# Kernel tuning notes

Hardware: AMD Instinct MI355X
Metric: run time of the kernel (lower is better)

Reference implementation:

```python
import jax, jax.numpy as jnp
import numpy as np

B, S, D, H = 2, 1536, 1024, 16
DK = D // H
NEG = -1e9
WEIGHT = 1.0  # undefined global `Weight` in source; treated as scalar 1.0


def setup_inputs() -> dict:
    key = jax.random.key(0)
    ks = jax.random.split(key, 16)
    inp = {
        "query": jax.random.normal(ks[0], (B, S, D), jnp.float32),
        "key": jax.random.normal(ks[1], (B, S, D), jnp.float32),
        "value": jax.random.normal(ks[2], (B, S, D), jnp.float32),
        "mask": jax.random.randint(ks[3], (B, 1, 1, S), 0, 2, jnp.int32),
        "mask1": jax.random.randint(ks[4], (B, 1, S, S), 0, 2, jnp.int32).astype(jnp.float32),
        "Wq": jax.random.normal(ks[5], (D, D), jnp.float32) / np.sqrt(D),
        "bq": jnp.zeros((D,), jnp.float32),
        "Wk": jax.random.normal(ks[6], (D, D), jnp.float32) / np.sqrt(D),
        "bk": jnp.zeros((D,), jnp.float32),
        "Wv": jax.random.normal(ks[7], (D, D), jnp.float32) / np.sqrt(D),
        "bv": jnp.zeros((D,), jnp.float32),
        "Wo": jax.random.normal(ks[8], (D, D), jnp.float32) / np.sqrt(D),
        "bo": jnp.zeros((D,), jnp.float32),
    }
    return inp


def _split_heads(x):
    # [B,S,D] -> [B,H,S,DK]
    return x.reshape(B, S, H, DK).transpose(0, 2, 1, 3)


def reference(query, key, value, mask, mask1, Wq, bq, Wk, bk, Wv, bv, Wo, bo):
    q = _split_heads(query @ Wq.T + bq)
    k = _split_heads(key @ Wk.T + bk)
    v = _split_heads(value @ Wv.T + bv)

    scores = jnp.einsum("bhqd,bhkd->bhqk", q, k) / jnp.sqrt(jnp.float32(DK))
    # softmax of mask1 over the query axis (dim=-2), zeros masked out
    m1 = jnp.where(mask1 == 0, NEG, mask1)
    m1s = jax.nn.softmax(m1, axis=-2)
    scores = (1.0 + m1s * mask1) * scores * WEIGHT
    scores = jnp.where(mask == 0, NEG, scores)
    p = jax.nn.softmax(scores, axis=-1)  # dropout: eval mode (identity)
    x = jnp.einsum("bhqk,bhkd->bhqd", p, v)
    x = x.transpose(0, 2, 1, 3).reshape(B, S, D)
    ret = x @ Wo.T + bo
    return ret, scores
```

## Files before the change

kernel.cpp:

```cpp
#include <hip/hip_runtime.h>
#include <hip/hip_bf16.h>

#define B_ 2
#define S_ 1536
#define D_ 1024
#define H_ 16
#define DK_ 64
#define KW_ 48
#define NT_ 24

#define RET_ELEMS 3145728
#define BITPACK_BLOCKS 18432

typedef __attribute__((ext_vector_type(8))) short short8;
typedef __attribute__((ext_vector_type(8))) unsigned short ushort8v;
typedef __attribute__((ext_vector_type(4))) unsigned short ushort4v;
typedef __attribute__((ext_vector_type(4))) float f32x4;

__device__ __forceinline__ unsigned short bf16_rne(float f) {
    return __builtin_bit_cast(unsigned short, __float2bfloat16(f));
}

struct CvtJobs {
    const float* src[7];
    unsigned short* dst[7];
};

__global__ __launch_bounds__(256) void preproc_kernel(
    const float* __restrict__ mask1, unsigned int* __restrict__ bits,
    float* __restrict__ colsum, CvtJobs j)
{
    const int blk = blockIdx.x;
    if (blk < BITPACK_BLOCKS) {
        if (blk < 12) colsum[blk * 256 + threadIdx.x] = 0.f;
        const size_t gid = (size_t)blk * 256 + threadIdx.x;
        const float v = mask1[gid];
        const unsigned long long bal = __ballot(v != 0.f);
        const int l = threadIdx.x & 63;
        if (l == 0)       bits[gid >> 5] = (unsigned int)bal;
        else if (l == 32) bits[gid >> 5] = (unsigned int)(bal >> 32);
        return;
    }
    int rb = blk - BITPACK_BLOCKS;
    int job, base;
    if (rb < 4608) { job = rb / 1536; base = rb % 1536; }
    else { rb -= 4608; job = 3 + rb / 512; base = rb % 512; }
    const size_t i = ((size_t)base * 256 + threadIdx.x) * 8;
    const float* s = j.src[job] + i;
    float4 f0 = *(const float4*)s;
    float4 f1 = *(const float4*)(s + 4);
    ushort8v u;
    u[0]=bf16_rne(f0.x); u[1]=bf16_rne(f0.y); u[2]=bf16_rne(f0.z); u[3]=bf16_rne(f0.w);
    u[4]=bf16_rne(f1.x); u[5]=bf16_rne(f1.y); u[6]=bf16_rne(f1.z); u[7]=bf16_rne(f1.w);
    *(ushort8v*)(j.dst[job] + i) = u;
}

__global__ void colcount_bits_kernel(const unsigned int* __restrict__ bits, float* __restrict__ colsum) {
    const int b     = blockIdx.x / 6;
    const int chunk = blockIdx.x % 6;
    const int col   = chunk * 256 + threadIdx.x;
    const int q0    = blockIdx.y * 96;
    const int wword = col >> 5, bit = col & 31;
    const unsigned int* p = bits + ((size_t)b * S_ + q0) * KW_ + wword;
    int s = 0;
    #pragma unroll 8
    for (int q = 0; q < 96; ++q) s += (p[(size_t)q * KW_] >> bit) & 1u;
    atomicAdd(&colsum[b * S_ + col], (float)s);
}

struct Proj { const unsigned short* A; const unsigned short* W; const float* bias; unsigned short* C; };

__global__ __launch_bounds__(512) void qkv_gemm_kernel(Proj p0, Proj p1, Proj p2) {
    const int bid = blockIdx.x;
    const int xcd = bid & 7, idx = bid >> 3;
    const int zy = xcd * 9 + (idx >> 3);
    const int bx = idx & 7;
    const int z = zy / 24, by = zy % 24;

    const unsigned short* A = z == 0 ? p0.A    : (z == 1 ? p1.A    : p2.A);
    const unsigned short* W = z == 0 ? p0.W    : (z == 1 ? p1.W    : p2.W);
    const float* bias       = z == 0 ? p0.bias : (z == 1 ? p1.bias : p2.bias);
    unsigned short* C       = z == 0 ? p0.C    : (z == 1 ? p1.C    : p2.C);

    __shared__ unsigned short As[128][72];
    __shared__ unsigned short Bs[128][72];
    const int tid = threadIdx.x;
    const int w = tid >> 6, lane = tid & 63;
    const int g = lane >> 4, c = lane & 15;
    const int wm = w >> 2, wn = w & 3;
    const int m0 = by * 128, n0 = bx * 128;
    const int trow = tid >> 2;
    const int tcol = (tid & 3) * 16;

    f32x4 acc[4][2];
    #pragma unroll
    for (int m = 0; m < 4; ++m)
        #pragma unroll
        for (int n = 0; n < 2; ++n)
            acc[m][n] = f32x4{0.f, 0.f, 0.f, 0.f};

    for (int k0 = 0; k0 < D_; k0 += 64) {
        {
            const unsigned short* ap = A + (size_t)(m0 + trow) * D_ + k0 + tcol;
            *(ushort8v*)&As[trow][tcol]     = *(const ushort8v*)ap;
            *(ushort8v*)&As[trow][tcol + 8] = *(const ushort8v*)(ap + 8);
            const unsigned short* wp = W + (size_t)(n0 + trow) * D_ + k0 + tcol;
            *(ushort8v*)&Bs[trow][tcol]     = *(const ushort8v*)wp;
            *(ushort8v*)&Bs[trow][tcol + 8] = *(const ushort8v*)(wp + 8);
        }
        __syncthreads();
        #pragma unroll
        for (int kk = 0; kk < 2; ++kk) {
            short8 a[4], bb[2];
            #pragma unroll
            for (int m = 0; m < 4; ++m) a[m]  = *(const short8*)&As[wm * 64 + m * 16 + c][kk * 32 + g * 8];
            #pragma unroll
            for (int n = 0; n < 2; ++n) bb[n] = *(const short8*)&Bs[wn * 32 + n * 16 + c][kk * 32 + g * 8];
            __builtin_amdgcn_s_setprio(1);
            #pragma unroll
            for (int m = 0; m < 4; ++m)
                #pragma unroll
                for (int n = 0; n < 2; ++n)
                    acc[m][n] = __builtin_amdgcn_mfma_f32_16x16x32_bf16(a[m], bb[n], acc[m][n], 0, 0, 0);
            __builtin_amdgcn_s_setprio(0);
        }
        __syncthreads();
    }
    #pragma unroll
    for (int n = 0; n < 2; ++n) {
        const int col = n0 + wn * 32 + n * 16 + c;
        const float bval = bias[col];
        #pragma unroll
        for (int m = 0; m < 4; ++m) {
            const int row0 = m0 + wm * 64 + m * 16 + g * 4;
            #pragma unroll
            for (int r = 0; r < 4; ++r)
                C[(size_t)(row0 + r) * D_ + col] = bf16_rne(acc[m][n][r] + bval);
        }
    }
}

__global__ __launch_bounds__(256) void out_gemm_kernel(
    const unsigned short* __restrict__ A, const unsigned short* __restrict__ W,
    const float* __restrict__ bias, float* __restrict__ C)
{
    const int bid = blockIdx.x;
    const int xcd = bid & 7, idx = bid >> 3;
    const int yg = xcd * 6 + (idx >> 4);
    const int bx = idx & 15;

    __shared__ unsigned short As[64][72];
    __shared__ unsigned short Bs[64][72];
    const int tid = threadIdx.x;
    const int w = tid >> 6, lane = tid & 63;
    const int g = lane >> 4, c = lane & 15;
    const int wm = w >> 1, wn = w & 1;
    const int m0 = yg * 64, n0 = bx * 64;
    const int trow = tid >> 2;
    const int tcol = (tid & 3) * 16;

    f32x4 acc[2][2];
    #pragma unroll
    for (int m = 0; m < 2; ++m)
        #pragma unroll
        for (int n = 0; n < 2; ++n)
            acc[m][n] = f32x4{0.f, 0.f, 0.f, 0.f};

    for (int k0 = 0; k0 < D_; k0 += 64) {
        {
            const unsigned short* ap = A + (size_t)(m0 + trow) * D_ + k0 + tcol;
            *(ushort8v*)&As[trow][tcol]     = *(const ushort8v*)ap;
            *(ushort8v*)&As[trow][tcol + 8] = *(const ushort8v*)(ap + 8);
            const unsigned short* wp = W + (size_t)(n0 + trow) * D_ + k0 + tcol;
            *(ushort8v*)&Bs[trow][tcol]     = *(const ushort8v*)wp;
            *(ushort8v*)&Bs[trow][tcol + 8] = *(const ushort8v*)(wp + 8);
        }
        __syncthreads();
        #pragma unroll
        for (int kk = 0; kk < 2; ++kk) {
            short8 a[2], bb[2];
            #pragma unroll
            for (int m = 0; m < 2; ++m) a[m]  = *(const short8*)&As[wm * 32 + m * 16 + c][kk * 32 + g * 8];
            #pragma unroll
            for (int n = 0; n < 2; ++n) bb[n] = *(const short8*)&Bs[wn * 32 + n * 16 + c][kk * 32 + g * 8];
            __builtin_amdgcn_s_setprio(1);
            #pragma unroll
            for (int m = 0; m < 2; ++m)
                #pragma unroll
                for (int n = 0; n < 2; ++n)
                    acc[m][n] = __builtin_amdgcn_mfma_f32_16x16x32_bf16(a[m], bb[n], acc[m][n], 0, 0, 0);
            __builtin_amdgcn_s_setprio(0);
        }
        __syncthreads();
    }
    #pragma unroll
    for (int n = 0; n < 2; ++n) {
        const int col = n0 + wn * 32 + n * 16 + c;
        const float bval = bias[col];
        #pragma unroll
        for (int m = 0; m < 2; ++m) {
            const int row0 = m0 + wm * 32 + m * 16 + g * 4;
            #pragma unroll
            for (int r = 0; r < 4; ++r)
                C[(size_t)(row0 + r) * D_ + col] = acc[m][n][r] + bval;
        }
    }
}

__global__ __launch_bounds__(256) void attn_kernel(
    const unsigned short* __restrict__ Qb, const unsigned short* __restrict__ Kb,
    const unsigned short* __restrict__ Vb, const int* __restrict__ mask,
    const unsigned int* __restrict__ bits, const float* __restrict__ colsum,
    float* __restrict__ scores, unsigned short* __restrict__ X)
{
    const int bid = blockIdx.x;
    const int xcd = bid & 7, idx = bid >> 3;
    const int grp = xcd * 4 + idx / 24;
    const int qt  = idx % 24;
    const int h = grp & 15, b = grp >> 4;

    const int tid = threadIdx.x;
    const int w = tid >> 6, lane = tid & 63;
    const int g = lane >> 4, c = lane & 15;

    __shared__ unsigned short VT_lds[2][64][72];
    __shared__ unsigned short P_lds[4][16][72];
    __shared__ float fac_lds[S_];

    for (int i = tid; i < S_; i += 256) {
        const int km = mask[b * S_ + i];
        const float cnt = colsum[b * S_ + i];
        fac_lds[i] = (km == 0) ? -1.f : ((cnt > 0.f) ? (1.f / cnt) : 0.f);
    }

    const int qrow0 = qt * 64 + w * 16;
    const unsigned short* qptr = Qb + ((size_t)b * S_ + qrow0 + c) * D_ + h * DK_;
    const short8 qf0 = *(const short8*)(qptr + g * 8);
    const short8 qf1 = *(const short8*)(qptr + 32 + g * 8);

    float mrow = -INFINITY, lrow = 0.f;
    f32x4 o[4];
    #pragma unroll
    for (int n = 0; n < 4; ++n) o[n] = f32x4{0.f, 0.f, 0.f, 0.f};

    float* srow = scores + ((((size_t)(b * H_ + h)) * S_ + qrow0 + c) * S_);
    const unsigned int* brow = bits + ((size_t)b * S_ + qrow0 + c) * KW_;
    const int kr = tid & 63, half = tid >> 6;
    const unsigned short* vrow = Vb + ((size_t)b * S_ + kr) * D_ + h * DK_ + half * 16;

    {
        short8 v0 = *(const short8*)vrow;
        short8 v1 = *(const short8*)(vrow + 8);
        #pragma unroll
        for (int j = 0; j < 8; ++j) {
            VT_lds[0][half * 16 + j][kr]     = (unsigned short)v0[j];
            VT_lds[0][half * 16 + 8 + j][kr] = (unsigned short)v1[j];
        }
    }
    __syncthreads();

    for (int kt = 0; kt < NT_; ++kt) {
        const int k0 = kt * 64;
        const int cur = kt & 1;
        const bool have_next = (kt + 1) < NT_;

        short8 nv0, nv1;
        if (have_next) {
            const unsigned short* vs = vrow + (size_t)(k0 + 64) * D_;
            nv0 = *(const short8*)vs;
            nv1 = *(const short8*)(vs + 8);
        }

        f32x4 sacc[4];
        #pragma unroll
        for (int n = 0; n < 4; ++n) sacc[n] = f32x4{0.f, 0.f, 0.f, 0.f};
        short8 kf0[4], kf1[4];
        #pragma unroll
        for (int n = 0; n < 4; ++n) {
            const unsigned short* kp = Kb + ((size_t)b * S_ + k0 + n * 16 + c) * D_ + h * DK_;
            kf0[n] = *(const short8*)(kp + g * 8);
            kf1[n] = *(const short8*)(kp + 32 + g * 8);
        }
        __builtin_amdgcn_s_setprio(1);
        #pragma unroll
        for (int n = 0; n < 4; ++n) {
            sacc[n] = __builtin_amdgcn_mfma_f32_16x16x32_bf16(kf0[n], qf0, sacc[n], 0, 0, 0);
            sacc[n] = __builtin_amdgcn_mfma_f32_16x16x32_bf16(kf1[n], qf1, sacc[n], 0, 0, 0);
        }
        __builtin_amdgcn_s_setprio(0);

        const unsigned int w0 = brow[(k0 >> 5)];
        const unsigned int w1 = brow[(k0 >> 5) + 1];
        float pmax = -INFINITY;
        f32x4 sv[4];
        #pragma unroll
        for (int n = 0; n < 4; ++n) {
            const f32x4 fv = *(const f32x4*)&fac_lds[k0 + n * 16 + g * 4];
            const unsigned int wsel = (n < 2) ? w0 : w1;
            #pragma unroll
            for (int r = 0; r < 4; ++r) {
                const int kl = n * 16 + g * 4 + r;
                const float f = fv[r];
                const float icnt = fmaxf(f, 0.f);
                const float bit = (float)((wsel >> (kl & 31)) & 1u);
                float s = sacc[n][r] * 0.125f * (1.f + bit * icnt);
                s = (f < 0.f) ? -1e9f : s;
                sv[n][r] = s;
                pmax = fmaxf(pmax, s);
            }
            __builtin_nontemporal_store(sv[n], (f32x4*)&srow[k0 + n * 16 + g * 4]);
        }

        pmax = fmaxf(pmax, __shfl_xor(pmax, 16));
        pmax = fmaxf(pmax, __shfl_xor(pmax, 32));
        const float nm = fmaxf(mrow, pmax);
        const float scq = __expf(mrow - nm);
        mrow = nm;
        lrow *= scq;
        float sc_o[4];
        #pragma unroll
        for (int r = 0; r < 4; ++r) sc_o[r] = __shfl(scq, (lane & 48) | (g * 4 + r));
        #pragma unroll
        for (int n = 0; n < 4; ++n)
            #pragma unroll
            for (int r = 0; r < 4; ++r) o[n][r] *= sc_o[r];

        #pragma unroll
        for (int n = 0; n < 4; ++n) {
            ushort4v pu;
            #pragma unroll
            for (int r = 0; r < 4; ++r) {
                const float p = __expf(sv[n][r] - mrow);
                lrow += p;
                pu[r] = bf16_rne(p);
            }
            *(ushort4v*)&P_lds[w][c][n * 16 + g * 4] = pu;
        }

        if (have_next) {
            #pragma unroll
            for (int j = 0; j < 8; ++j) {
                VT_lds[cur ^ 1][half * 16 + j][kr]     = (unsigned short)nv0[j];
                VT_lds[cur ^ 1][half * 16 + 8 + j][kr] = (unsigned short)nv1[j];
            }
        }

        __builtin_amdgcn_s_setprio(1);
        #pragma unroll
        for (int kk = 0; kk < 2; ++kk) {
            const short8 pa = *(const short8*)&P_lds[w][c][kk * 32 + g * 8];
            #pragma unroll
            for (int n = 0; n < 4; ++n) {
                const short8 vf = *(const short8*)&VT_lds[cur][n * 16 + c][kk * 32 + g * 8];
                o[n] = __builtin_amdgcn_mfma_f32_16x16x32_bf16(pa, vf, o[n], 0, 0, 0);
            }
        }
        __builtin_amdgcn_s_setprio(0);
        __syncthreads();
    }

    lrow += __shfl_xor(lrow, 16);
    lrow += __shfl_xor(lrow, 32);
    const float linv = 1.f / lrow;
    float linv_o[4];
    #pragma unroll
    for (int r = 0; r < 4; ++r) linv_o[r] = __shfl(linv, (lane & 48) | (g * 4 + r));
    #pragma unroll
    for (int n = 0; n < 4; ++n)
        #pragma unroll
        for (int r = 0; r < 4; ++r) {
            const size_t idx = ((size_t)b * S_ + qrow0 + g * 4 + r) * D_ + h * DK_ + n * 16 + c;
            X[idx] = bf16_rne(o[n][r] * linv_o[r]);
        }
}

extern "C" void kernel_launch(void* const* d_in, const int* in_sizes, int n_in,
                              void* d_out, int out_size, void* d_ws, size_t ws_size,
                              hipStream_t stream) {
    const float* query = (const float*)d_in[0];
    const float* key   = (const float*)d_in[1];
    const float* value = (const float*)d_in[2];
    const int*   mask  = (const int*)d_in[3];
    const float* mask1 = (const float*)d_in[4];
    const float* Wq = (const float*)d_in[5];
    const float* bq = (const float*)d_in[6];
    const float* Wk = (const float*)d_in[7];
    const float* bk = (const float*)d_in[8];
    const float* Wv = (const float*)d_in[9];
    const float* bv = (const float*)d_in[10];
    const float* Wo = (const float*)d_in[11];
    const float* bo = (const float*)d_in[12];

    float* ret_out    = (float*)d_out;
    float* scores_out = ret_out + RET_ELEMS;

    const size_t SZ = (size_t)B_ * S_ * D_;
    const size_t WZ = (size_t)D_ * D_;
    float* colsum = (float*)d_ws;
    unsigned int* bits = (unsigned int*)((char*)d_ws + 16384);
    unsigned short* Qb  = (unsigned short*)((char*)d_ws + 16384 + 589824);
    unsigned short* Kb  = Qb + SZ;
    unsigned short* Vb  = Kb + SZ;
    unsigned short* Xb  = Vb + SZ;
    unsigned short* qf  = Xb + SZ;
    unsigned short* kf  = qf + SZ;
    unsigned short* vf  = kf + SZ;
    unsigned short* Wqb = vf + SZ;
    unsigned short* Wkb = Wqb + WZ;
    unsigned short* Wvb = Wkb + WZ;
    unsigned short* Wob = Wvb + WZ;

    CvtJobs jobs;
    jobs.src[0] = query; jobs.dst[0] = qf;
    jobs.src[1] = key;   jobs.dst[1] = kf;
    jobs.src[2] = value; jobs.dst[2] = vf;
    jobs.src[3] = Wq;    jobs.dst[3] = Wqb;
    jobs.src[4] = Wk;    jobs.dst[4] = Wkb;
    jobs.src[5] = Wv;    jobs.dst[5] = Wvb;
    jobs.src[6] = Wo;    jobs.dst[6] = Wob;

    preproc_kernel<<<BITPACK_BLOCKS + 3 * 1536 + 4 * 512, 256, 0, stream>>>(mask1, bits, colsum, jobs);
    colcount_bits_kernel<<<dim3(12, 16), 256, 0, stream>>>(bits, colsum);

    Proj p0{qf, Wqb, bq, Qb}, p1{kf, Wkb, bk, Kb}, p2{vf, Wvb, bv, Vb};
    qkv_gemm_kernel<<<576, 512, 0, stream>>>(p0, p1, p2);

    attn_kernel<<<768, 256, 0, stream>>>(Qb, Kb, Vb, mask, bits, colsum, scores_out, Xb);

    out_gemm_kernel<<<768, 256, 0, stream>>>(Xb, Wob, bo, ret_out);
}
```

Measured before the change: 201.6 us.

## Prefetch K tiles in attention, fuse column count into QKV GEMM, retile GEMM

The attention loop is unrolled by two, and the K fragments for the next tile are loaded into registers while the current tile is computed, so global load latency is hidden. The online softmax now computes exponentials against the previous running max and rescales them afterwards, starting the running max at zero. The standalone column-count kernel is folded into extra blocks of the QKV GEMM launch, removing one launch. The QKV GEMM is retiled to 96x128 tiles with 384 threads and a different wave layout. The costs are higher register pressure from the double-buffered K fragments, and a risk of exp overflow if scores were ever large, because the running max starts at zero instead of minus infinity.

```diff
diff --git a/kernel.cpp b/kernel.cpp
--- a/kernel.cpp
+++ b/kernel.cpp
@@ -11,6 +11,7 @@
 
 #define RET_ELEMS 3145728
 #define BITPACK_BLOCKS 18432
+#define QKV_BLOCKS 768
 
 typedef __attribute__((ext_vector_type(8))) short short8;
 typedef __attribute__((ext_vector_type(8))) unsigned short ushort8v;
@@ -55,84 +56,97 @@
     *(ushort8v*)(j.dst[job] + i) = u;
 }
 
-__global__ void colcount_bits_kernel(const unsigned int* __restrict__ bits, float* __restrict__ colsum) {
-    const int b     = blockIdx.x / 6;
-    const int chunk = blockIdx.x % 6;
-    const int col   = chunk * 256 + threadIdx.x;
-    const int q0    = blockIdx.y * 96;
-    const int wword = col >> 5, bit = col & 31;
-    const unsigned int* p = bits + ((size_t)b * S_ + q0) * KW_ + wword;
-    int s = 0;
-    #pragma unroll 8
-    for (int q = 0; q < 96; ++q) s += (p[(size_t)q * KW_] >> bit) & 1u;
-    atomicAdd(&colsum[b * S_ + col], (float)s);
-}
-
 struct Proj { const unsigned short* A; const unsigned short* W; const float* bias; unsigned short* C; };
 
-__global__ __launch_bounds__(512) void qkv_gemm_kernel(Proj p0, Proj p1, Proj p2) {
+__global__ __launch_bounds__(384) void qkv_gemm_kernel(
+    Proj p0, Proj p1, Proj p2,
+    const unsigned int* __restrict__ bits, float* __restrict__ colsum)
+{
     const int bid = blockIdx.x;
+    const int tid = threadIdx.x;
+
+    if (bid >= QKV_BLOCKS) {
+        const int id2 = bid - QKV_BLOCKS;
+        const int b = id2 / 96, rest = id2 % 96;
+        const int q0 = (rest >> 2) * 64;
+        const int col = (rest & 3) * 384 + tid;
+        const int wword = col >> 5, bit = col & 31;
+        const unsigned int* p = bits + ((size_t)b * S_ + q0) * KW_ + wword;
+        int s = 0;
+        #pragma unroll 8
+        for (int q = 0; q < 64; ++q) s += (p[(size_t)q * KW_] >> bit) & 1u;
+        atomicAdd(&colsum[b * S_ + col], (float)s);
+        return;
+    }
+
     const int xcd = bid & 7, idx = bid >> 3;
-    const int zy = xcd * 9 + (idx >> 3);
+    const int zm = xcd * 12 + (idx >> 3);
     const int bx = idx & 7;
-    const int z = zy / 24, by = zy % 24;
+    const int z = zm / 32, by = zm % 32;
 
     const unsigned short* A = z == 0 ? p0.A    : (z == 1 ? p1.A    : p2.A);
     const unsigned short* W = z == 0 ? p0.W    : (z == 1 ? p1.W    : p2.W);
     const float* bias       = z == 0 ? p0.bias : (z == 1 ? p1.bias : p2.bias);
     unsigned short* C       = z == 0 ? p0.C    : (z == 1 ? p1.C    : p2.C);
 
-    __shared__ unsigned short As[128][72];
+    __shared__ unsigned short As[96][72];
     __shared__ unsigned short Bs[128][72];
-    const int tid = threadIdx.x;
     const int w = tid >> 6, lane = tid & 63;
     const int g = lane >> 4, c = lane & 15;
-    const int wm = w >> 2, wn = w & 3;
-    const int m0 = by * 128, n0 = bx * 128;
-    const int trow = tid >> 2;
-    const int tcol = (tid & 3) * 16;
-
-    f32x4 acc[4][2];
-    #pragma unroll
-    for (int m = 0; m < 4; ++m)
-        #pragma unroll
-        for (int n = 0; n < 2; ++n)
+    const int wm = w >> 1, wn = w & 1;
+    const int m0 = by * 96, n0 = bx * 128;
+    const int trowA = tid >> 2;
+    const int tcolA = (tid & 3) * 16;
+
+    f32x4 acc[2][4];
+    #pragma unroll
+    for (int m = 0; m < 2; ++m)
+        #pragma unroll
+        for (int n = 0; n < 4; ++n)
             acc[m][n] = f32x4{0.f, 0.f, 0.f, 0.f};
 
     for (int k0 = 0; k0 < D_; k0 += 64) {
         {
-            const unsigned short* ap = A + (size_t)(m0 + trow) * D_ + k0 + tcol;
-            *(ushort8v*)&As[trow][tcol]     = *(const ushort8v*)ap;
-            *(ushort8v*)&As[trow][tcol + 8] = *(const ushort8v*)(ap + 8);
-            const unsigned short* wp = W + (size_t)(n0 + trow) * D_ + k0 + tcol;
-            *(ushort8v*)&Bs[trow][tcol]     = *(const ushort8v*)wp;
-            *(ushort8v*)&Bs[trow][tcol + 8] = *(const ushort8v*)(wp + 8);
+            const unsigned short* ap = A + (size_t)(m0 + trowA) * D_ + k0 + tcolA;
+            *(ushort8v*)&As[trowA][tcolA]     = *(const ushort8v*)ap;
+            *(ushort8v*)&As[trowA][tcolA + 8] = *(const ushort8v*)(ap + 8);
+            const int r1 = tid >> 2, c1 = (tid & 3) * 16;
+            const unsigned short* wp = W + (size_t)(n0 + r1) * D_ + k0 + c1;
+            *(ushort8v*)&Bs[r1][c1]     = *(const ushort8v*)wp;
+            *(ushort8v*)&Bs[r1][c1 + 8] = *(const ushort8v*)(wp + 8);
+            if (tid < 128) {
+                const int c2i = 384 + tid;
+                const int r2 = c2i >> 2, c2 = (c2i & 3) * 16;
+                const unsigned short* wp2 = W + (size_t)(n0 + r2) * D_ + k0 + c2;
+                *(ushort8v*)&Bs[r2][c2]     = *(const ushort8v*)wp2;
+                *(ushort8v*)&Bs[r2][c2 + 8] = *(const ushort8v*)(wp2 + 8);
+            }
         }
         __syncthreads();
         #pragma unroll
         for (int kk = 0; kk < 2; ++kk) {
-            short8 a[4], bb[2];
-            #pragma unroll
-            for (int m = 0; m < 4; ++m) a[m]  = *(const short8*)&As[wm * 64 + m * 16 + c][kk * 32 + g * 8];
-            #pragma unroll
-            for (int n = 0; n < 2; ++n) bb[n] = *(const short8*)&Bs[wn * 32 + n * 16 + c][kk * 32 + g * 8];
+            short8 a[2], bb[4];
+            #pragma unroll
+            for (int m = 0; m < 2; ++m) a[m]  = *(const short8*)&As[wm * 32 + m * 16 + c][kk * 32 + g * 8];
+            #pragma unroll
+            for (int n = 0; n < 4; ++n) bb[n] = *(const short8*)&Bs[wn * 64 + n * 16 + c][kk * 32 + g * 8];
             __builtin_amdgcn_s_setprio(1);
             #pragma unroll
-            for (int m = 0; m < 4; ++m)
+            for (int m = 0; m < 2; ++m)
                 #pragma unroll
-                for (int n = 0; n < 2; ++n)
+                for (int n = 0; n < 4; ++n)
                     acc[m][n] = __builtin_amdgcn_mfma_f32_16x16x32_bf16(a[m], bb[n], acc[m][n], 0, 0, 0);
             __builtin_amdgcn_s_setprio(0);
         }
         __syncthreads();
     }
     #pragma unroll
-    for (int n = 0; n < 2; ++n) {
-        const int col = n0 + wn * 32 + n * 16 + c;
+    for (int n = 0; n < 4; ++n) {
+        const int col = n0 + wn * 64 + n * 16 + c;
         const float bval = bias[col];
         #pragma unroll
-        for (int m = 0; m < 4; ++m) {
-            const int row0 = m0 + wm * 64 + m * 16 + g * 4;
+        for (int m = 0; m < 2; ++m) {
+            const int row0 = m0 + wm * 32 + m * 16 + g * 4;
             #pragma unroll
             for (int r = 0; r < 4; ++r)
                 C[(size_t)(row0 + r) * D_ + col] = bf16_rne(acc[m][n][r] + bval);
@@ -238,7 +252,7 @@
     const short8 qf0 = *(const short8*)(qptr + g * 8);
     const short8 qf1 = *(const short8*)(qptr + 32 + g * 8);
 
-    float mrow = -INFINITY, lrow = 0.f;
+    float mrow = 0.f, lrow = 0.f;
     f32x4 o[4];
     #pragma unroll
     for (int n = 0; n < 4; ++n) o[n] = f32x4{0.f, 0.f, 0.f, 0.f};
@@ -247,6 +261,7 @@
     const unsigned int* brow = bits + ((size_t)b * S_ + qrow0 + c) * KW_;
     const int kr = tid & 63, half = tid >> 6;
     const unsigned short* vrow = Vb + ((size_t)b * S_ + kr) * D_ + h * DK_ + half * 16;
+    const unsigned short* kbase = Kb + ((size_t)b * S_ + c) * D_ + h * DK_;
 
     {
         short8 v0 = *(const short8*)vrow;
@@ -257,107 +272,115 @@
             VT_lds[0][half * 16 + 8 + j][kr] = (unsigned short)v1[j];
         }
     }
+    short8 ka0[4], ka1[4], kb0[4], kb1[4];
+    #pragma unroll
+    for (int n = 0; n < 4; ++n) {
+        const unsigned short* kp = kbase + (size_t)(n * 16) * D_;
+        ka0[n] = *(const short8*)(kp + g * 8);
+        ka1[n] = *(const short8*)(kp + 32 + g * 8);
+    }
     __syncthreads();
 
-    for (int kt = 0; kt < NT_; ++kt) {
-        const int k0 = kt * 64;
-        const int cur = kt & 1;
-        const bool have_next = (kt + 1) < NT_;
-
-        short8 nv0, nv1;
-        if (have_next) {
-            const unsigned short* vs = vrow + (size_t)(k0 + 64) * D_;
-            nv0 = *(const short8*)vs;
-            nv1 = *(const short8*)(vs + 8);
-        }
-
-        f32x4 sacc[4];
-        #pragma unroll
-        for (int n = 0; n < 4; ++n) sacc[n] = f32x4{0.f, 0.f, 0.f, 0.f};
-        short8 kf0[4], kf1[4];
-        #pragma unroll
-        for (int n = 0; n < 4; ++n) {
-            const unsigned short* kp = Kb + ((size_t)b * S_ + k0 + n * 16 + c) * D_ + h * DK_;
-            kf0[n] = *(const short8*)(kp + g * 8);
-            kf1[n] = *(const short8*)(kp + 32 + g * 8);
-        }
-        __builtin_amdgcn_s_setprio(1);
-        #pragma unroll
-        for (int n = 0; n < 4; ++n) {
-            sacc[n] = __builtin_amdgcn_mfma_f32_16x16x32_bf16(kf0[n], qf0, sacc[n], 0, 0, 0);
-            sacc[n] = __builtin_amdgcn_mfma_f32_16x16x32_bf16(kf1[n], qf1, sacc[n], 0, 0, 0);
-        }
-        __builtin_amdgcn_s_setprio(0);
-
-        const unsigned int w0 = brow[(k0 >> 5)];
-        const unsigned int w1 = brow[(k0 >> 5) + 1];
-        float pmax = -INFINITY;
-        f32x4 sv[4];
-        #pragma unroll
-        for (int n = 0; n < 4; ++n) {
-            const f32x4 fv = *(const f32x4*)&fac_lds[k0 + n * 16 + g * 4];
-            const unsigned int wsel = (n < 2) ? w0 : w1;
-            #pragma unroll
-            for (int r = 0; r < 4; ++r) {
-                const int kl = n * 16 + g * 4 + r;
-                const float f = fv[r];
-                const float icnt = fmaxf(f, 0.f);
-                const float bit = (float)((wsel >> (kl & 31)) & 1u);
-                float s = sacc[n][r] * 0.125f * (1.f + bit * icnt);
-                s = (f < 0.f) ? -1e9f : s;
-                sv[n][r] = s;
-                pmax = fmaxf(pmax, s);
-            }
-            __builtin_nontemporal_store(sv[n], (f32x4*)&srow[k0 + n * 16 + g * 4]);
-        }
-
-        pmax = fmaxf(pmax, __shfl_xor(pmax, 16));
-        pmax = fmaxf(pmax, __shfl_xor(pmax, 32));
-        const float nm = fmaxf(mrow, pmax);
-        const float scq = __expf(mrow - nm);
-        mrow = nm;
-        lrow *= scq;
-        float sc_o[4];
-        #pragma unroll
-        for (int r = 0; r < 4; ++r) sc_o[r] = __shfl(scq, (lane & 48) | (g * 4 + r));
-        #pragma unroll
-        for (int n = 0; n < 4; ++n)
-            #pragma unroll
-            for (int r = 0; r < 4; ++r) o[n][r] *= sc_o[r];
-
-        #pragma unroll
-        for (int n = 0; n < 4; ++n) {
-            ushort4v pu;
-            #pragma unroll
-            for (int r = 0; r < 4; ++r) {
-                const float p = __expf(sv[n][r] - mrow);
-                lrow += p;
-                pu[r] = bf16_rne(p);
-            }
-            *(ushort4v*)&P_lds[w][c][n * 16 + g * 4] = pu;
-        }
-
-        if (have_next) {
-            #pragma unroll
-            for (int j = 0; j < 8; ++j) {
-                VT_lds[cur ^ 1][half * 16 + j][kr]     = (unsigned short)nv0[j];
-                VT_lds[cur ^ 1][half * 16 + 8 + j][kr] = (unsigned short)nv1[j];
-            }
-        }
-
-        __builtin_amdgcn_s_setprio(1);
-        #pragma unroll
-        for (int kk = 0; kk < 2; ++kk) {
-            const short8 pa = *(const short8*)&P_lds[w][c][kk * 32 + g * 8];
-            #pragma unroll
-            for (int n = 0; n < 4; ++n) {
-                const short8 vf = *(const short8*)&VT_lds[cur][n * 16 + c][kk * 32 + g * 8];
-                o[n] = __builtin_amdgcn_mfma_f32_16x16x32_bf16(pa, vf, o[n], 0, 0, 0);
-            }
-        }
-        __builtin_amdgcn_s_setprio(0);
-        __syncthreads();
-    }
+#define TILE_BODY(KT, CUR, KC0, KC1, KN0, KN1)                                              \
+    {                                                                                        \
+        const int k0 = (KT) * 64;                                                            \
+        const bool have_next = (KT) + 1 < NT_;                                               \
+        short8 nv0, nv1;                                                                     \
+        if (have_next) {                                                                     \
+            const unsigned short* vs = vrow + (size_t)(k0 + 64) * D_;                        \
+            nv0 = *(const short8*)vs;                                                        \
+            nv1 = *(const short8*)(vs + 8);                                                  \
+            _Pragma("unroll")                                                                \
+            for (int n = 0; n < 4; ++n) {                                                    \
+                const unsigned short* kp = kbase + (size_t)(k0 + 64 + n * 16) * D_;          \
+                KN0[n] = *(const short8*)(kp + g * 8);                                       \
+                KN1[n] = *(const short8*)(kp + 32 + g * 8);                                  \
+            }                                                                                \
+        }                                                                                    \
+        f32x4 sacc[4];                                                                       \
+        _Pragma("unroll")                                                                    \
+        for (int n = 0; n < 4; ++n) sacc[n] = f32x4{0.f, 0.f, 0.f, 0.f};                     \
+        __builtin_amdgcn_s_setprio(1);                                                       \
+        _Pragma("unroll")                                                                    \
+        for (int n = 0; n < 4; ++n) {                                                        \
+            sacc[n] = __builtin_amdgcn_mfma_f32_16x16x32_bf16(KC0[n], qf0, sacc[n], 0, 0, 0);\
+            sacc[n] = __builtin_amdgcn_mfma_f32_16x16x32_bf16(KC1[n], qf1, sacc[n], 0, 0, 0);\
+        }                                                                                    \
+        __builtin_amdgcn_s_setprio(0);                                                       \
+        const unsigned int w0 = brow[(k0 >> 5)];                                             \
+        const unsigned int w1 = brow[(k0 >> 5) + 1];                                         \
+        float pmax = -INFINITY;                                                              \
+        float p[4][4];                                                                       \
+        _Pragma("unroll")                                                                    \
+        for (int n = 0; n < 4; ++n) {                                                        \
+            const f32x4 fv = *(const f32x4*)&fac_lds[k0 + n * 16 + g * 4];                   \
+            const unsigned int wsel = (n < 2) ? w0 : w1;                                     \
+            f32x4 sv;                                                                        \
+            _Pragma("unroll")                                                                \
+            for (int r = 0; r < 4; ++r) {                                                    \
+                const int kl = n * 16 + g * 4 + r;                                           \
+                const float f = fv[r];                                                       \
+                const float icnt = fmaxf(f, 0.f);                                            \
+                const float bit = (float)((wsel >> (kl & 31)) & 1u);                         \
+                float s = sacc[n][r] * 0.125f * (1.f + bit * icnt);                          \
+                s = (f < 0.f) ? -1e9f : s;                                                   \
+                sv[r] = s;                                                                   \
+                pmax = fmaxf(pmax, s);                                                       \
+                p[n][r] = __expf(s - mrow);              \
+            }                                                                                \
+            __builtin_nontemporal_store(sv, (f32x4*)&srow[k0 + n * 16 + g * 4]);             \
+        }                                                                                    \
+        pmax = fmaxf(pmax, __shfl_xor(pmax, 16));                                            \
+        pmax = fmaxf(pmax, __shfl_xor(pmax, 32));                                            \
+        const float nm = fmaxf(mrow, pmax);                                                  \
+        const float scq = __expf(mrow - nm);                                                 \
+        mrow = nm;                                                                           \
+        float psum = 0.f;                                                                    \
+        _Pragma("unroll")                                                                    \
+        for (int n = 0; n < 4; ++n)                                                          \
+            _Pragma("unroll")                                                                \
+            for (int r = 0; r < 4; ++r) psum += p[n][r];                                     \
+        lrow = (lrow + psum) * scq;                                                          \
+        float sc_o[4];                                                                       \
+        _Pragma("unroll")                                                                    \
+        for (int r = 0; r < 4; ++r) sc_o[r] = __shfl(scq, (lane & 48) | (g * 4 + r));        \
+        _Pragma("unroll")                                                                    \
+        for (int n = 0; n < 4; ++n)                                                          \
+            _Pragma("unroll")                                                                \
+            for (int r = 0; r < 4; ++r) o[n][r] *= sc_o[r];                                  \
+        _Pragma("unroll")                                                                    \
+        for (int n = 0; n < 4; ++n) {                                                        \
+            ushort4v pu;                                                                     \
+            _Pragma("unroll")                                                                \
+            for (int r = 0; r < 4; ++r) pu[r] = bf16_rne(p[n][r] * scq);                     \
+            *(ushort4v*)&P_lds[w][c][n * 16 + g * 4] = pu;                                   \
+        }                                                                                    \
+        if (have_next) {                                                                     \
+            _Pragma("unroll")                                                                \
+            for (int j = 0; j < 8; ++j) {                                                    \
+                VT_lds[(CUR) ^ 1][half * 16 + j][kr]     = (unsigned short)nv0[j];           \
+                VT_lds[(CUR) ^ 1][half * 16 + 8 + j][kr] = (unsigned short)nv1[j];           \
+            }                                                                                \
+        }                                                                                    \
+        __builtin_amdgcn_s_setprio(1);                                                       \
+        _Pragma("unroll")                                                                    \
+        for (int kk = 0; kk < 2; ++kk) {                                                     \
+            const short8 pa = *(const short8*)&P_lds[w][c][kk * 32 + g * 8];                 \
+            _Pragma("unroll")                                                                \
+            for (int n = 0; n < 4; ++n) {                                                    \
+                const short8 vf = *(const short8*)&VT_lds[CUR][n * 16 + c][kk * 32 + g * 8]; \
+                o[n] = __builtin_amdgcn_mfma_f32_16x16x32_bf16(pa, vf, o[n], 0, 0, 0);       \
+            }                                                                                \
+        }                                                                                    \
+        __builtin_amdgcn_s_setprio(0);                                                       \
+        __syncthreads();                                                                     \
+    }
+
+    for (int kt2 = 0; kt2 < NT_; kt2 += 2) {
+        TILE_BODY(kt2,     0, ka0, ka1, kb0, kb1)
+        TILE_BODY(kt2 + 1, 1, kb0, kb1, ka0, ka1)
+    }
+#undef TILE_BODY
 
     lrow += __shfl_xor(lrow, 16);
     lrow += __shfl_xor(lrow, 32);
@@ -369,8 +392,8 @@
     for (int n = 0; n < 4; ++n)
         #pragma unroll
         for (int r = 0; r < 4; ++r) {
-            const size_t idx = ((size_t)b * S_ + qrow0 + g * 4 + r) * D_ + h * DK_ + n * 16 + c;
-            X[idx] = bf16_rne(o[n][r] * linv_o[r]);
+            const size_t idx2 = ((size_t)b * S_ + qrow0 + g * 4 + r) * D_ + h * DK_ + n * 16 + c;
+            X[idx2] = bf16_rne(o[n][r] * linv_o[r]);
         }
 }
 
@@ -420,10 +443,9 @@
     jobs.src[6] = Wo;    jobs.dst[6] = Wob;
 
     preproc_kernel<<<BITPACK_BLOCKS + 3 * 1536 + 4 * 512, 256, 0, stream>>>(mask1, bits, colsum, jobs);
-    colcount_bits_kernel<<<dim3(12, 16), 256, 0, stream>>>(bits, colsum);
 
     Proj p0{qf, Wqb, bq, Qb}, p1{kf, Wkb, bk, Kb}, p2{vf, Wvb, bv, Vb};
-    qkv_gemm_kernel<<<576, 512, 0, stream>>>(p0, p1, p2);
+    qkv_gemm_kernel<<<QKV_BLOCKS + 192, 384, 0, stream>>>(p0, p1, p2, bits, colsum);
 
     attn_kernel<<<768, 256, 0, stream>>>(Qb, Kb, Vb, mask, bits, colsum, scores_out, Xb);
 
```

Measured after the change: 217.9 us, median of 2. 8.1% more time.

## Fold column-count into QKV GEMM launch and retile GEMM to 96x128 blocks

Applied to the files above, without the earlier changes.

Removes the separate column-count kernel and runs its work as 192 extra trailing blocks of the QKV GEMM launch, saving one kernel launch and letting the small job overlap with GEMM tiles. The QKV GEMM is retiled from 128x128 tiles with 512 threads to 96x128 tiles with 384 threads (6 waves, 2x4 MFMA per wave), which gives 768 blocks instead of 576 for better CU fill and tail balance. The XCD block swizzle is updated to match. Risks include smaller per-block reuse, an uneven B-tile load split across threads, and colcount blocks competing with GEMM blocks for CUs.

```diff
diff --git a/kernel.cpp b/kernel.cpp
--- a/kernel.cpp
+++ b/kernel.cpp
@@ -11,6 +11,7 @@
 
 #define RET_ELEMS 3145728
 #define BITPACK_BLOCKS 18432
+#define QKV_BLOCKS 768
 
 typedef __attribute__((ext_vector_type(8))) short short8;
 typedef __attribute__((ext_vector_type(8))) unsigned short ushort8v;
@@ -55,84 +56,97 @@
     *(ushort8v*)(j.dst[job] + i) = u;
 }
 
-__global__ void colcount_bits_kernel(const unsigned int* __restrict__ bits, float* __restrict__ colsum) {
-    const int b     = blockIdx.x / 6;
-    const int chunk = blockIdx.x % 6;
-    const int col   = chunk * 256 + threadIdx.x;
-    const int q0    = blockIdx.y * 96;
-    const int wword = col >> 5, bit = col & 31;
-    const unsigned int* p = bits + ((size_t)b * S_ + q0) * KW_ + wword;
-    int s = 0;
-    #pragma unroll 8
-    for (int q = 0; q < 96; ++q) s += (p[(size_t)q * KW_] >> bit) & 1u;
-    atomicAdd(&colsum[b * S_ + col], (float)s);
-}
-
 struct Proj { const unsigned short* A; const unsigned short* W; const float* bias; unsigned short* C; };
 
-__global__ __launch_bounds__(512) void qkv_gemm_kernel(Proj p0, Proj p1, Proj p2) {
+__global__ __launch_bounds__(384) void qkv_gemm_kernel(
+    Proj p0, Proj p1, Proj p2,
+    const unsigned int* __restrict__ bits, float* __restrict__ colsum)
+{
     const int bid = blockIdx.x;
+    const int tid = threadIdx.x;
+
+    if (bid >= QKV_BLOCKS) {
+        const int id2 = bid - QKV_BLOCKS;
+        const int b = id2 / 96, rest = id2 % 96;
+        const int q0 = (rest >> 2) * 64;
+        const int col = (rest & 3) * 384 + tid;
+        const int wword = col >> 5, bit = col & 31;
+        const unsigned int* p = bits + ((size_t)b * S_ + q0) * KW_ + wword;
+        int s = 0;
+        #pragma unroll 8
+        for (int q = 0; q < 64; ++q) s += (p[(size_t)q * KW_] >> bit) & 1u;
+        atomicAdd(&colsum[b * S_ + col], (float)s);
+        return;
+    }
+
     const int xcd = bid & 7, idx = bid >> 3;
-    const int zy = xcd * 9 + (idx >> 3);
+    const int zm = xcd * 12 + (idx >> 3);
     const int bx = idx & 7;
-    const int z = zy / 24, by = zy % 24;
+    const int z = zm / 32, by = zm % 32;
 
     const unsigned short* A = z == 0 ? p0.A    : (z == 1 ? p1.A    : p2.A);
     const unsigned short* W = z == 0 ? p0.W    : (z == 1 ? p1.W    : p2.W);
     const float* bias       = z == 0 ? p0.bias : (z == 1 ? p1.bias : p2.bias);
     unsigned short* C       = z == 0 ? p0.C    : (z == 1 ? p1.C    : p2.C);
 
-    __shared__ unsigned short As[128][72];
+    __shared__ unsigned short As[96][72];
     __shared__ unsigned short Bs[128][72];
-    const int tid = threadIdx.x;
     const int w = tid >> 6, lane = tid & 63;
     const int g = lane >> 4, c = lane & 15;
-    const int wm = w >> 2, wn = w & 3;
-    const int m0 = by * 128, n0 = bx * 128;
-    const int trow = tid >> 2;
-    const int tcol = (tid & 3) * 16;
-
-    f32x4 acc[4][2];
-    #pragma unroll
-    for (int m = 0; m < 4; ++m)
-        #pragma unroll
-        for (int n = 0; n < 2; ++n)
+    const int wm = w >> 1, wn = w & 1;
+    const int m0 = by * 96, n0 = bx * 128;
+    const int trowA = tid >> 2;
+    const int tcolA = (tid & 3) * 16;
+
+    f32x4 acc[2][4];
+    #pragma unroll
+    for (int m = 0; m < 2; ++m)
+        #pragma unroll
+        for (int n = 0; n < 4; ++n)
             acc[m][n] = f32x4{0.f, 0.f, 0.f, 0.f};
 
     for (int k0 = 0; k0 < D_; k0 += 64) {
         {
-            const unsigned short* ap = A + (size_t)(m0 + trow) * D_ + k0 + tcol;
-            *(ushort8v*)&As[trow][tcol]     = *(const ushort8v*)ap;
-            *(ushort8v*)&As[trow][tcol + 8] = *(const ushort8v*)(ap + 8);
-            const unsigned short* wp = W + (size_t)(n0 + trow) * D_ + k0 + tcol;
-            *(ushort8v*)&Bs[trow][tcol]     = *(const ushort8v*)wp;
-            *(ushort8v*)&Bs[trow][tcol + 8] = *(const ushort8v*)(wp + 8);
+            const unsigned short* ap = A + (size_t)(m0 + trowA) * D_ + k0 + tcolA;
+            *(ushort8v*)&As[trowA][tcolA]     = *(const ushort8v*)ap;
+            *(ushort8v*)&As[trowA][tcolA + 8] = *(const ushort8v*)(ap + 8);
+            const int r1 = tid >> 2, c1 = (tid & 3) * 16;
+            const unsigned short* wp = W + (size_t)(n0 + r1) * D_ + k0 + c1;
+            *(ushort8v*)&Bs[r1][c1]     = *(const ushort8v*)wp;
+            *(ushort8v*)&Bs[r1][c1 + 8] = *(const ushort8v*)(wp + 8);
+            if (tid < 128) {
+                const int c2i = 384 + tid;
+                const int r2 = c2i >> 2, c2 = (c2i & 3) * 16;
+                const unsigned short* wp2 = W + (size_t)(n0 + r2) * D_ + k0 + c2;
+                *(ushort8v*)&Bs[r2][c2]     = *(const ushort8v*)wp2;
+                *(ushort8v*)&Bs[r2][c2 + 8] = *(const ushort8v*)(wp2 + 8);
+            }
         }
         __syncthreads();
         #pragma unroll
         for (int kk = 0; kk < 2; ++kk) {
-            short8 a[4], bb[2];
-            #pragma unroll
-            for (int m = 0; m < 4; ++m) a[m]  = *(const short8*)&As[wm * 64 + m * 16 + c][kk * 32 + g * 8];
-            #pragma unroll
-            for (int n = 0; n < 2; ++n) bb[n] = *(const short8*)&Bs[wn * 32 + n * 16 + c][kk * 32 + g * 8];
+            short8 a[2], bb[4];
+            #pragma unroll
+            for (int m = 0; m < 2; ++m) a[m]  = *(const short8*)&As[wm * 32 + m * 16 + c][kk * 32 + g * 8];
+            #pragma unroll
+            for (int n = 0; n < 4; ++n) bb[n] = *(const short8*)&Bs[wn * 64 + n * 16 + c][kk * 32 + g * 8];
             __builtin_amdgcn_s_setprio(1);
             #pragma unroll
-            for (int m = 0; m < 4; ++m)
+            for (int m = 0; m < 2; ++m)
                 #pragma unroll
-                for (int n = 0; n < 2; ++n)
+                for (int n = 0; n < 4; ++n)
                     acc[m][n] = __builtin_amdgcn_mfma_f32_16x16x32_bf16(a[m], bb[n], acc[m][n], 0, 0, 0);
             __builtin_amdgcn_s_setprio(0);
         }
         __syncthreads();
     }
     #pragma unroll
-    for (int n = 0; n < 2; ++n) {
-        const int col = n0 + wn * 32 + n * 16 + c;
+    for (int n = 0; n < 4; ++n) {
+        const int col = n0 + wn * 64 + n * 16 + c;
         const float bval = bias[col];
         #pragma unroll
-        for (int m = 0; m < 4; ++m) {
-            const int row0 = m0 + wm * 64 + m * 16 + g * 4;
+        for (int m = 0; m < 2; ++m) {
+            const int row0 = m0 + wm * 32 + m * 16 + g * 4;
             #pragma unroll
             for (int r = 0; r < 4; ++r)
                 C[(size_t)(row0 + r) * D_ + col] = bf16_rne(acc[m][n][r] + bval);
@@ -369,8 +383,8 @@
     for (int n = 0; n < 4; ++n)
         #pragma unroll
         for (int r = 0; r < 4; ++r) {
-            const size_t idx = ((size_t)b * S_ + qrow0 + g * 4 + r) * D_ + h * DK_ + n * 16 + c;
-            X[idx] = bf16_rne(o[n][r] * linv_o[r]);
+            const size_t idx2 = ((size_t)b * S_ + qrow0 + g * 4 + r) * D_ + h * DK_ + n * 16 + c;
+            X[idx2] = bf16_rne(o[n][r] * linv_o[r]);
         }
 }
 
@@ -420,10 +434,9 @@
     jobs.src[6] = Wo;    jobs.dst[6] = Wob;
 
     preproc_kernel<<<BITPACK_BLOCKS + 3 * 1536 + 4 * 512, 256, 0, stream>>>(mask1, bits, colsum, jobs);
-    colcount_bits_kernel<<<dim3(12, 16), 256, 0, stream>>>(bits, colsum);
 
     Proj p0{qf, Wqb, bq, Qb}, p1{kf, Wkb, bk, Kb}, p2{vf, Wvb, bv, Vb};
-    qkv_gemm_kernel<<<576, 512, 0, stream>>>(p0, p1, p2);
+    qkv_gemm_kernel<<<QKV_BLOCKS + 192, 384, 0, stream>>>(p0, p1, p2, bits, colsum);
 
     attn_kernel<<<768, 256, 0, stream>>>(Qb, Kb, Vb, mask, bits, colsum, scores_out, Xb);
 
```

Measured after the change: 204.5 us. No clear change (+1.5%).
